# Performance work log

Measured on AMD Instinct MI355X. Metric: run time of the kernel, lower is better.

## Reference

```python
import jax, jax.numpy as jnp
import numpy as np

H = 128; F = 64; G = 50; L = 4; CUT = 10.0
M = 256; K = 8; A = 32
N_TOPO = M * A; N = M * K * A; NCONF = M * K
E_CONF = N * 16; E_GRAPH = N_TOPO * 4
ATOM_TYPES = 100; BOND_TYPES = 10
OFFSETS = jnp.linspace(0.0, CUT, G)
GCOEFF = -0.5 / (CUT / (G - 1)) ** 2  # GaussianSmearing coeff
BN_EPS = 1e-5


def batchnorm(x, g, b):
    # BatchNorm1d in training mode: batch statistics over nodes
    mu = x.mean(0)
    var = ((x - mu) ** 2).mean(0)
    return (x - mu) * jax.lax.rsqrt(var + BN_EPS) * g + b


def setup_inputs():
    key = jax.random.key(0)
    ks = jax.random.split(key, 20)
    s = lambda k, shp: (jax.random.normal(k, shp) * 0.05).astype(jnp.float32)
    inp = {}
    inp["x_topo"] = jax.random.randint(ks[0], (N_TOPO,), 0, ATOM_TYPES)
    inp["pos"] = jax.random.normal(ks[1], (N, 3), dtype=jnp.float32) * 3.0
    inp["edge_index_conf"] = jax.random.randint(ks[2], (2, E_CONF), 0, N)
    inp["edge_index_graph"] = jax.random.randint(ks[3], (2, E_GRAPH), 0, N_TOPO)
    inp["edge_attr_graph"] = jax.random.randint(ks[4], (E_GRAPH,), 0, BOND_TYPES)
    # conf_node_batch: for molecule i, repeat arange(A)+i*A over K conformers
    cnb = (np.arange(M)[:, None, None] * A + np.broadcast_to(np.arange(A), (K, A))).reshape(-1)
    inp["conf_node_batch"] = jnp.asarray(cnb, dtype=jnp.int32)
    inp["pos_batch"] = jnp.repeat(jnp.arange(NCONF), A).astype(jnp.int32)
    inp["conf_batch"] = jnp.repeat(jnp.arange(M), K).astype(jnp.int32)
    # parameters
    inp["atom_emb"] = s(ks[5], (ATOM_TYPES, H))
    inp["cf_lin1_w"] = s(ks[6], (L, H, F))
    inp["cf_mlp_w1"] = s(ks[7], (L, G, F)); inp["cf_mlp_b1"] = jnp.zeros((L, F), jnp.float32)
    inp["cf_mlp_w2"] = s(ks[8], (L, F, F)); inp["cf_mlp_b2"] = jnp.zeros((L, F), jnp.float32)
    inp["cf_lin2_w"] = s(ks[9], (L, F, H)); inp["cf_lin2_b"] = jnp.zeros((L, H), jnp.float32)
    inp["lin_w"] = s(ks[10], (L, H, H)); inp["lin_b"] = jnp.zeros((L, H), jnp.float32)
    inp["bond_emb"] = s(ks[11], (L, BOND_TYPES, H))
    inp["gin_w1"] = s(ks[12], (L, H, H)); inp["gin_b1"] = jnp.zeros((L, H), jnp.float32)
    inp["gin_w2"] = s(ks[13], (L, H, H)); inp["gin_b2"] = jnp.zeros((L, H), jnp.float32)
    inp["gin_bn_g"] = jnp.ones((L, H), jnp.float32); inp["gin_bn_b"] = jnp.zeros((L, H), jnp.float32)
    inp["bn_g"] = jnp.ones((L, H), jnp.float32); inp["bn_b"] = jnp.zeros((L, H), jnp.float32)
    inp["gin_eps"] = jnp.zeros((L,), jnp.float32)
    inp["out_w1"] = s(ks[14], (H, H)); inp["out_b1"] = jnp.zeros((H,), jnp.float32)
    inp["out_w2"] = s(ks[15], (H, 1)); inp["out_b2"] = jnp.zeros((1,), jnp.float32)
    return inp


def _forward(x_topo, edge_index_conf, edge_index_graph, edge_attr_graph,
             conf_node_batch, pos_batch, conf_batch,
             pos, atom_emb, cf_lin1_w, cf_mlp_w1, cf_mlp_b1, cf_mlp_w2, cf_mlp_b2,
             cf_lin2_w, cf_lin2_b, lin_w, lin_b, bond_emb,
             gin_w1, gin_b1, gin_w2, gin_b2, gin_bn_g, gin_bn_b, bn_g, bn_b,
             gin_eps, out_w1, out_b1, out_w2, out_b2):
    # AtomEncoder on topo graph, broadcast to all conformers
    x = atom_emb[x_topo][conf_node_batch]                      # [N, H]
    row, col = edge_index_conf[0], edge_index_conf[1]
    d = pos[row] - pos[col]
    ew = jnp.sqrt(jnp.sum(d * d, axis=-1) + 1e-12)             # edge_weight_conf [E_conf]
    ea = jnp.exp(GCOEFF * (ew[:, None] - OFFSETS) ** 2)        # GaussianSmearing [E_conf, G]
    cwin = 0.5 * (jnp.cos(ew * jnp.pi / CUT) + 1.0)            # SchNet cosine cutoff
    gr, gc = edge_index_graph[0], edge_index_graph[1]
    for l in range(L):
        # CFConv branch (use_conf)
        Wf = (jax.nn.relu(ea @ cf_mlp_w1[l] + cf_mlp_b1[l]) @ cf_mlp_w2[l] + cf_mlp_b2[l]) * cwin[:, None]
        h = x @ cf_lin1_w[l]                                   # lin1, no bias
        agg = jax.ops.segment_sum(h[row] * Wf, col, num_segments=N)
        h = agg @ cf_lin2_w[l] + cf_lin2_b[l]                  # lin2
        h = jax.nn.relu(h)
        h = h @ lin_w[l] + lin_b[l]
        out = x + h                                            # residual
        # GIN branch on topo graph (use_graph)
        x_agg = jax.ops.segment_max(x, conf_node_batch, num_segments=N_TOPO)
        eemb = bond_emb[l][edge_attr_graph]                    # BondEncoder
        magg = jax.ops.segment_sum(jax.nn.relu(x_agg[gr] + eemb), gc, num_segments=N_TOPO)
        hg = (1.0 + gin_eps[l]) * x_agg + magg
        hg = jax.nn.relu(batchnorm(hg @ gin_w1[l] + gin_b1[l], gin_bn_g[l], gin_bn_b[l]))
        hg = hg @ gin_w2[l] + gin_b2[l]
        hg = batchnorm(hg, bn_g[l], bn_b[l])
        out = out + hg[conf_node_batch]
        x = jax.nn.relu(out)
    x = jax.ops.segment_max(x, pos_batch, num_segments=NCONF)  # pool atoms -> conformers
    x = jax.ops.segment_max(x, conf_batch, num_segments=M)     # pool conformers -> molecules
    x = jax.nn.relu(x @ out_w1 + out_b1) @ out_w2 + out_b2     # out_layer
    return x                                                   # training mode: no clamp


def reference(x_topo, pos, edge_index_conf, edge_index_graph, edge_attr_graph,
              conf_node_batch, pos_batch, conf_batch,
              atom_emb, cf_lin1_w, cf_mlp_w1, cf_mlp_b1, cf_mlp_w2, cf_mlp_b2,
              cf_lin2_w, cf_lin2_b, lin_w, lin_b, bond_emb,
              gin_w1, gin_b1, gin_w2, gin_b2, gin_bn_g, gin_bn_b, bn_g, bn_b,
              gin_eps, out_w1, out_b1, out_w2, out_b2):
    return _forward(x_topo, edge_index_conf, edge_index_graph, edge_attr_graph,
                    conf_node_batch, pos_batch, conf_batch,
                    pos, atom_emb, cf_lin1_w, cf_mlp_w1, cf_mlp_b1, cf_mlp_w2, cf_mlp_b2,
                    cf_lin2_w, cf_lin2_b, lin_w, lin_b, bond_emb,
                    gin_w1, gin_b1, gin_w2, gin_b2, gin_bn_g, gin_bn_b, bn_g, bn_b,
                    gin_eps, out_w1, out_b1, out_w2, out_b2)
```

## Files before the change

kernel.cpp:

```cpp
#include <hip/hip_runtime.h>
#include <hip/hip_bf16.h>

#define EC 1048576
#define NN 65536
#define NT 8192
#define MM 256
#define HH 128
#define FF 64
#define GG 50
#define EG 32768

#define TBL 2048
#define TBL_SHIFT 11
#define TRANGE 14.0f

#define CAP 32
#define OVF_CAP 8192
#define NEB (NN * 64 / 256)
#define SEB (8 * (EC / 256))

#define SENT 0xFFE00000

constexpr float STEP = 10.0f / 49.0f;
constexpr float GC = -0.5f / (STEP * STEP);

typedef __attribute__((ext_vector_type(8))) short bf16x8;
typedef __attribute__((ext_vector_type(4))) float f32x4;

__device__ __forceinline__ ushort f2b(float v) {
    __hip_bfloat16 h = __float2bfloat16(v);
    return *(ushort*)&h;
}
__device__ __forceinline__ float b2f(ushort u) {
    return __uint_as_float(((unsigned)u) << 16);
}

#define SETUP_B0 (EC / 256)
#define SETUP_B1 (SETUP_B0 + EG / 256)
#define SETUP_B2 (SETUP_B1 + NN * HH / 8 / 256)
#define SETUP_B3 (SETUP_B2 + NN * CAP / 4 / 256)
__global__ __launch_bounds__(256) void setup_kernel(
    const int* __restrict__ eic, const int* __restrict__ cnb,
    const int* __restrict__ eig, const float* __restrict__ pos,
    const float* __restrict__ emb, const int* __restrict__ xtopo,
    int* __restrict__ degC, ushort* __restrict__ uu16, ushort* __restrict__ xb,
    int4* __restrict__ pay_pad4)
{
    int b = blockIdx.x, tid = threadIdx.x;
    if (b < SETUP_B0) {
        int e = b * 256 + tid;
        int r = eic[e], c = eic[EC + e];
        float dx = pos[r*3+0] - pos[c*3+0];
        float dy = pos[r*3+1] - pos[c*3+1];
        float dz = pos[r*3+2] - pos[c*3+2];
        float w = sqrtf(dx*dx + dy*dy + dz*dz + 1e-12f);
        float u = fminf(w * ((TBL - 1) / TRANGE), 2046.96875f);
        uu16[e] = (ushort)(int)(u * 32.0f);
    } else if (b < SETUP_B1) {
        atomicAdd(&degC[eig[EG + (b - SETUP_B0) * 256 + tid]], 1);
    } else if (b < SETUP_B2) {
        int idx = (b - SETUP_B1) * 256 + tid;
        int n = idx >> 4;
        int f8 = (idx & 15) << 3;
        const float* e = emb + (size_t)xtopo[cnb[n]] * HH + f8;
        float4 v0 = *(const float4*)e;
        float4 v1 = *(const float4*)(e + 4);
        ushort u[8] = {f2b(v0.x), f2b(v0.y), f2b(v0.z), f2b(v0.w),
                       f2b(v1.x), f2b(v1.y), f2b(v1.z), f2b(v1.w)};
        *(bf16x8*)(xb + ((size_t)idx << 3)) = *(const bf16x8*)u;
    } else {
        int idx = (b - SETUP_B2) * 256 + tid;
        pay_pad4[idx] = make_int4(SENT, SENT, SENT, SENT);
    }
}

__global__ __launch_bounds__(256) void scanC_kernel(
    const int* __restrict__ degC, int* __restrict__ offsC, int* __restrict__ curC)
{
    __shared__ int s[256];
    __shared__ int base;
    int tid = threadIdx.x;
    if (tid == 0) base = 0;
    __syncthreads();
    for (int c = 0; c < NT / 256; c++) {
        int v = degC[c * 256 + tid];
        s[tid] = v;
        __syncthreads();
        for (int off = 1; off < 256; off <<= 1) {
            int t = (tid >= off) ? s[tid - off] : 0;
            __syncthreads();
            s[tid] += t;
            __syncthreads();
        }
        int excl = s[tid] - v + base;
        offsC[c * 256 + tid] = excl;
        curC[c * 256 + tid] = excl;
        __syncthreads();
        if (tid == 255) base += s[255];
        __syncthreads();
    }
    if (tid == 0) offsC[NT] = EG;
}

__global__ __launch_bounds__(256) void scatter_all_kernel(
    const int* __restrict__ eic, const ushort* __restrict__ uu16,
    const int* __restrict__ eig, const int* __restrict__ eattr,
    int* __restrict__ cntA, int* __restrict__ curC,
    int* __restrict__ pay_pad, int2* __restrict__ gpay,
    int* __restrict__ ovf_cnt, int2* __restrict__ ovf)
{
    int b = blockIdx.x, tid = threadIdx.x;
    if (b < SEB) {
        int part = b & 7;
        int e = (b >> 3) * 256 + tid;
        int c = eic[EC + e];
        if ((c >> 13) != part) return;
        int pay = ((int)uu16[e] << 16) | (eic[e] & 0xFFFF);
        int slot = atomicAdd(&cntA[c], 1);
        if (slot < CAP) {
            pay_pad[c * CAP + slot] = pay;
        } else {
            int o = atomicAdd(ovf_cnt, 1);
            if (o < OVF_CAP) ovf[o] = make_int2(c, pay);
        }
    } else {
        int e = (b - SEB) * 256 + tid;
        int p = atomicAdd(&curC[eig[EG + e]], 1);
        gpay[p] = make_int2(eig[e], eattr[e]);
    }
}

__global__ __launch_bounds__(64) void build_table_kernel(
    const float* __restrict__ w1a, const float* __restrict__ b1a,
    const float* __restrict__ w2a, const float* __restrict__ b2a,
    float* __restrict__ table_all)
{
    int l = blockIdx.x >> TBL_SHIFT;
    int p = blockIdx.x & (TBL - 1);
    int lane = threadIdx.x;
    const float* w1 = w1a + (size_t)l * GG * FF;
    const float* b1 = b1a + (size_t)l * FF;
    const float* w2 = w2a + (size_t)l * FF * FF;
    const float* b2 = b2a + (size_t)l * FF;
    float w = p * (TRANGE / (TBL - 1));
    float t = b1[lane];
    for (int g = 0; g < GG; g++) {
        float d = w - g * STEP;
        float ea = __expf(GC * d * d);
        t = fmaf(ea, w1[g * 64 + lane], t);
    }
    __shared__ float ts[64];
    ts[lane] = fmaxf(t, 0.f);
    __syncthreads();
    float wf = b2[lane];
    for (int i = 0; i < 64; i++)
        wf = fmaf(ts[i], w2[i * 64 + lane], wf);
    float cw = 0.5f * (__cosf(w * (3.14159265358979323846f / 10.0f)) + 1.0f);
    table_all[((size_t)l * TBL + p) * 64 + lane] = wf * cw;
}

__global__ __launch_bounds__(256) void pack_table_kernel(
    const float* __restrict__ table_all, ushort2* __restrict__ table2_all)
{
    int idx = blockIdx.x * 256 + threadIdx.x;
    int f = idx & 63;
    int rest = idx >> 6;
    int i = rest & (TBL - 1);
    int l = rest >> TBL_SHIFT;
    if (i == TBL - 1) {
        table2_all[idx] = make_ushort2(0, 0);
        return;
    }
    const float* T = table_all + ((size_t)l * TBL) * 64;
    float t0 = T[(size_t)i * 64 + f];
    float t1 = T[(size_t)(i + 1) * 64 + f];
    table2_all[idx] = make_ushort2(f2b(t0), f2b((t1 - t0) * 0.03125f));
}

__device__ __forceinline__ void prep_one(
    const float* __restrict__ W, ushort* __restrict__ Wf, int K, int N, int idx)
{
    int sz = K * N;
    int l = idx / sz;
    int t = idx - l * sz;
    int j = t & 7;
    int lane = (t >> 3) & 63;
    int rest = t >> 9;
    int KTl = K >> 5;
    int kt = rest % KTl;
    int nt = rest / KTl;
    int k = kt * 32 + (lane >> 4) * 8 + j;
    int n = nt * 16 + (lane & 15);
    Wf[idx] = f2b(W[(size_t)l * sz + (size_t)k * N + n]);
}

__global__ __launch_bounds__(256) void prep_all_kernel(
    const float* __restrict__ cf_lin1_w, const float* __restrict__ cf_lin2_w,
    const float* __restrict__ lin_w, const float* __restrict__ gin_w1,
    const float* __restrict__ gin_w2,
    ushort* __restrict__ w1f, ushort* __restrict__ w2f, ushort* __restrict__ wlf,
    ushort* __restrict__ gw1f, ushort* __restrict__ gw2f)
{
    int b = blockIdx.x, tid = threadIdx.x;
    if (b < 128)       prep_one(cf_lin1_w, w1f, HH, FF, b * 256 + tid);
    else if (b < 256)  prep_one(cf_lin2_w, w2f, FF, HH, (b - 128) * 256 + tid);
    else if (b < 512)  prep_one(lin_w, wlf, HH, HH, (b - 256) * 256 + tid);
    else if (b < 768)  prep_one(gin_w1, gw1f, HH, HH, (b - 512) * 256 + tid);
    else               prep_one(gin_w2, gw2f, HH, HH, (b - 768) * 256 + tid);
}

__global__ __launch_bounds__(256) void gemm_bf16_kernel(
    const ushort* __restrict__ A, const ushort* __restrict__ Bf,
    ushort* __restrict__ Cb)
{
    int tid = threadIdx.x;
    int wave = tid >> 6, lane = tid & 63;
    int m0 = (blockIdx.x * 4 + wave) * 16;
    int arow = m0 + (lane & 15);
    int ak = (lane >> 4) * 8;
    bf16x8 a[4];
    const ushort* Ap = A + (size_t)arow * 128 + ak;
    #pragma unroll
    for (int kt = 0; kt < 4; kt++)
        a[kt] = *(const bf16x8*)(Ap + kt * 32);
    f32x4 acc[4];
    #pragma unroll
    for (int i = 0; i < 4; i++) acc[i] = (f32x4){0.f, 0.f, 0.f, 0.f};
    const ushort* Bp = Bf + (size_t)lane * 8;
    #pragma unroll
    for (int nt = 0; nt < 4; nt++)
        #pragma unroll
        for (int kt = 0; kt < 4; kt++) {
            bf16x8 b = *(const bf16x8*)(Bp + ((size_t)(nt * 4 + kt)) * 512);
            acc[nt] = __builtin_amdgcn_mfma_f32_16x16x32_bf16(a[kt], b, acc[nt], 0, 0, 0);
        }
    int col0 = lane & 15;
    int rbase = m0 + (lane >> 4) * 4;
    #pragma unroll
    for (int nt = 0; nt < 4; nt++) {
        int col = nt * 16 + col0;
        #pragma unroll
        for (int r = 0; r < 4; r++)
            Cb[(size_t)(rbase + r) * 64 + col] = f2b(acc[nt][r]);
    }
}

#define EDGE8(BASE) { \
    int pq[8]; \
    { int4 q0 = *(const int4*)(pp + BASE); \
      int4 q1 = *(const int4*)(pp + BASE + 4); \
      pq[0]=__builtin_amdgcn_readfirstlane(q0.x); \
      pq[1]=__builtin_amdgcn_readfirstlane(q0.y); \
      pq[2]=__builtin_amdgcn_readfirstlane(q0.z); \
      pq[3]=__builtin_amdgcn_readfirstlane(q0.w); \
      pq[4]=__builtin_amdgcn_readfirstlane(q1.x); \
      pq[5]=__builtin_amdgcn_readfirstlane(q1.y); \
      pq[6]=__builtin_amdgcn_readfirstlane(q1.z); \
      pq[7]=__builtin_amdgcn_readfirstlane(q1.w); } \
    float h[8]; \
    _Pragma("unroll") \
    for (int q = 0; q < 8; q++) \
        h[q] = b2f(*(const ushort*)(h1c + ((((unsigned)(pq[q] & 0xFFFF)) << 7) + lane2))); \
    unsigned tt[8]; \
    _Pragma("unroll") \
    for (int q = 0; q < 8; q++) \
        tt[q] = *(const unsigned*)(tbc + (((((unsigned)pq[q]) >> 21) << 8) + lane4)); \
    _Pragma("unroll") \
    for (int q = 0; q < 8; q++) { \
        float fr = (float)((unsigned)((pq[q] >> 16) & 31)); \
        float t0 = __uint_as_float(tt[q] << 16); \
        float dts = __uint_as_float(tt[q] & 0xFFFF0000u); \
        float wf = fmaf(dts, fr, t0); \
        if (q & 1) acc1 = fmaf(h[q], wf, acc1); else acc0 = fmaf(h[q], wf, acc0); \
    } }

__global__ __launch_bounds__(256) void edge_xagg_kernel(
    const int* __restrict__ cntA, const int* __restrict__ pay_pad,
    const int* __restrict__ ovf_cnt, const int2* __restrict__ ovf,
    const ushort2* __restrict__ table2, const ushort* __restrict__ h1b,
    ushort* __restrict__ aggb,
    const ushort* __restrict__ xb, ushort* __restrict__ xaggb)
{
    int tid = threadIdx.x;
    if (blockIdx.x < NEB) {
        int lane = tid & 63;
        int node = __builtin_amdgcn_readfirstlane((blockIdx.x * 256 + tid) >> 6);
        unsigned lane2 = (unsigned)lane * 2;
        unsigned lane4 = (unsigned)lane * 4;
        const char* h1c = (const char*)h1b;
        const char* tbc = (const char*)table2;
        int deg = cntA[node];
        int n1 = min(deg, CAP);
        const int* pp = pay_pad + (size_t)node * CAP;
        float acc0 = 0.f, acc1 = 0.f;
        EDGE8(0);
        if (n1 > 8) {
            EDGE8(8);
            if (n1 > 16) {
                EDGE8(16);
                if (n1 > 24) EDGE8(24);
            }
        }
        float acc = acc0 + acc1;
        if (deg > CAP) {
            int no = min(*ovf_cnt, OVF_CAP);
            for (int j = 0; j < no; j++) {
                int2 o = ovf[j];
                if (o.x == node) {
                    unsigned uf = (unsigned)o.y >> 16;
                    int i0 = uf >> 5;
                    float fr = (float)(uf & 31);
                    ushort2 ttv = table2[(size_t)i0 * 64 + lane];
                    acc = fmaf(b2f(h1b[(size_t)(o.y & 0xFFFF) * 64 + lane]),
                               fmaf(b2f(ttv.y), fr, b2f(ttv.x)), acc);
                }
            }
        }
        aggb[(size_t)node * 64 + lane] = f2b(acc);
    } else {
        int idx = (blockIdx.x - NEB) * 256 + tid;
        int tn = idx >> 7, f = idx & 127;
        int m = tn >> 5, a = tn & 31;
        const ushort* base = xb + ((size_t)((m << 8) + a)) * HH + f;
        float mx = -3.4e38f;
        #pragma unroll
        for (int k = 0; k < 8; k++)
            mx = fmaxf(mx, b2f(base[(size_t)(k << 5) * HH]));
        xaggb[idx] = f2b(mx);
    }
}

#define TSTR 136

__global__ __launch_bounds__(256) void gin_gemm1_kernel(
    const int* __restrict__ goffs, const int2* __restrict__ gpay,
    const ushort* __restrict__ xaggb, const float* __restrict__ bemb,
    const float* __restrict__ eps, const ushort* __restrict__ Bf,
    const float* __restrict__ bias, ushort* __restrict__ Cb,
    float* __restrict__ gsum, float* __restrict__ gsq)
{
    __shared__ ushort hg0s[64 * TSTR];
    __shared__ float ssum[128], ssq[128];
    int tid = threadIdx.x;
    if (tid < 128) { ssum[tid] = 0.f; ssq[tid] = 0.f; }
    {
        int row = tid >> 2;
        int fc = (tid & 3) * 32;
        int tn = blockIdx.x * 64 + row;
        float e1 = 1.0f + eps[0];
        float acc[32];
        const ushort* xo = xaggb + (size_t)tn * HH + fc;
        #pragma unroll
        for (int c = 0; c < 4; c++) {
            bf16x8 x = *(const bf16x8*)(xo + c * 8);
            #pragma unroll
            for (int j = 0; j < 8; j++)
                acc[c * 8 + j] = e1 * b2f((ushort)x[j]);
        }
        int beg = goffs[tn], end = goffs[tn + 1];
        for (int p = beg; p < end; p++) {
            int2 g = gpay[p];
            const ushort* xs = xaggb + (size_t)g.x * HH + fc;
            const float* bs = bemb + (size_t)g.y * HH + fc;
            #pragma unroll
            for (int c = 0; c < 4; c++) {
                bf16x8 x = *(const bf16x8*)(xs + c * 8);
                float4 b0 = *(const float4*)(bs + c * 8);
                float4 b1 = *(const float4*)(bs + c * 8 + 4);
                float bb[8] = {b0.x, b0.y, b0.z, b0.w, b1.x, b1.y, b1.z, b1.w};
                #pragma unroll
                for (int j = 0; j < 8; j++)
                    acc[c * 8 + j] += fmaxf(b2f((ushort)x[j]) + bb[j], 0.f);
            }
        }
        ushort* dst = hg0s + row * TSTR + fc;
        #pragma unroll
        for (int j = 0; j < 32; j++) dst[j] = f2b(acc[j]);
    }
    __syncthreads();
    int wave = tid >> 6, lane = tid & 63;
    int lm = lane & 15, lq = lane >> 4;
    int ak = lq * 8;
    bf16x8 a[4];
    #pragma unroll
    for (int kt = 0; kt < 4; kt++)
        a[kt] = *(const bf16x8*)&hg0s[(wave * 16 + lm) * TSTR + ak + kt * 32];
    f32x4 acc[8];
    #pragma unroll
    for (int i = 0; i < 8; i++) acc[i] = (f32x4){0.f, 0.f, 0.f, 0.f};
    const ushort* Bp = Bf + (size_t)lane * 8;
    #pragma unroll
    for (int nt = 0; nt < 8; nt++)
        #pragma unroll
        for (int kt = 0; kt < 4; kt++) {
            bf16x8 b = *(const bf16x8*)(Bp + ((size_t)(nt * 4 + kt)) * 512);
            acc[nt] = __builtin_amdgcn_mfma_f32_16x16x32_bf16(a[kt], b, acc[nt], 0, 0, 0);
        }
    int rbase = blockIdx.x * 64 + wave * 16 + lq * 4;
    #pragma unroll
    for (int nt = 0; nt < 8; nt++) {
        int col = nt * 16 + lm;
        float bs = bias[col];
        float ps = 0.f, pq = 0.f;
        #pragma unroll
        for (int r = 0; r < 4; r++) {
            float v = acc[nt][r] + bs;
            Cb[(size_t)(rbase + r) * 128 + col] = f2b(v);
            ps += v; pq += v * v;
        }
        atomicAdd(&ssum[col], ps);
        atomicAdd(&ssq[col], pq);
    }
    __syncthreads();
    if (tid < 128) {
        atomicAdd(&gsum[tid], ssum[tid]);
        atomicAdd(&gsq[tid], ssq[tid]);
    }
}

__global__ __launch_bounds__(256) void gemm_bn_stats_kernel(
    const ushort* __restrict__ Araw, const float* __restrict__ sum1,
    const float* __restrict__ sq1, const float* __restrict__ g1,
    const float* __restrict__ bb1, const ushort* __restrict__ Bf,
    const float* __restrict__ bias, ushort* __restrict__ Cb,
    float* __restrict__ gsum, float* __restrict__ gsq)
{
    __shared__ float ssum[128], ssq[128];
    int tid = threadIdx.x;
    if (tid < 128) { ssum[tid] = 0.f; ssq[tid] = 0.f; }
    __syncthreads();
    int wave = tid >> 6, lane = tid & 63;
    int m0 = (blockIdx.x * 4 + wave) * 16;
    int arow = m0 + (lane & 15);
    int ak = (lane >> 4) * 8;
    const float INV_NT = 1.0f / NT;
    bf16x8 a[4];
    const ushort* Ap = Araw + (size_t)arow * 128 + ak;
    #pragma unroll
    for (int kt = 0; kt < 4; kt++) {
        bf16x8 raw = *(const bf16x8*)(Ap + kt * 32);
        ushort ub[8];
        #pragma unroll
        for (int j = 0; j < 8; j++) {
            int k = ak + kt * 32 + j;
            float mu = sum1[k] * INV_NT;
            float var = sq1[k] * INV_NT - mu * mu;
            float inv = rsqrtf(var + 1e-5f);
            float w = fmaxf((b2f((ushort)raw[j]) - mu) * inv * g1[k] + bb1[k], 0.f);
            ub[j] = f2b(w);
        }
        a[kt] = *(bf16x8*)ub;
    }
    f32x4 acc[8];
    #pragma unroll
    for (int i = 0; i < 8; i++) acc[i] = (f32x4){0.f, 0.f, 0.f, 0.f};
    const ushort* Bp = Bf + (size_t)lane * 8;
    #pragma unroll
    for (int nt = 0; nt < 8; nt++)
        #pragma unroll
        for (int kt = 0; kt < 4; kt++) {
            bf16x8 b = *(const bf16x8*)(Bp + ((size_t)(nt * 4 + kt)) * 512);
            acc[nt] = __builtin_amdgcn_mfma_f32_16x16x32_bf16(a[kt], b, acc[nt], 0, 0, 0);
        }
    int col0 = lane & 15;
    int rbase = m0 + (lane >> 4) * 4;
    #pragma unroll
    for (int nt = 0; nt < 8; nt++) {
        int col = nt * 16 + col0;
        float bs = bias[col];
        float ps = 0.f, pq = 0.f;
        #pragma unroll
        for (int r = 0; r < 4; r++) {
            float v = acc[nt][r] + bs;
            Cb[(size_t)(rbase + r) * 128 + col] = f2b(v);
            ps += v; pq += v * v;
        }
        atomicAdd(&ssum[col], ps);
        atomicAdd(&ssq[col], pq);
    }
    __syncthreads();
    if (tid < 128) {
        atomicAdd(&gsum[tid], ssum[tid]);
        atomicAdd(&gsq[tid], ssq[tid]);
    }
}

__global__ __launch_bounds__(256) void fused_lin_kernel(
    const ushort* __restrict__ aggb, const ushort* __restrict__ w2,
    const float* __restrict__ b2, const ushort* __restrict__ w3,
    const float* __restrict__ b3, const ushort* __restrict__ hgBb,
    const float* __restrict__ sum2, const float* __restrict__ sq2,
    const float* __restrict__ g2, const float* __restrict__ bb2,
    const int* __restrict__ cnb, const ushort* __restrict__ w1n,
    ushort* __restrict__ xb, ushort* __restrict__ h1b)
{
    __shared__ ushort t1s[4][16 * TSTR];
    __shared__ ushort t2s[4][16 * TSTR];
    int tid = threadIdx.x;
    int wave = tid >> 6, lane = tid & 63;
    int m0 = (blockIdx.x * 4 + wave) * 16;
    int lm = lane & 15;
    int lq = lane >> 4;
    ushort* T1 = t1s[wave];
    ushort* T2 = t2s[wave];
    const float INV_NT = 1.0f / NT;

    const ushort* Ap = aggb + (size_t)(m0 + lm) * 64 + lq * 8;
    bf16x8 a1[2];
    a1[0] = *(const bf16x8*)(Ap);
    a1[1] = *(const bf16x8*)(Ap + 32);
    f32x4 acc[8];
    #pragma unroll
    for (int i = 0; i < 8; i++) acc[i] = (f32x4){0.f, 0.f, 0.f, 0.f};
    {
        const ushort* Bp = w2 + (size_t)lane * 8;
        #pragma unroll
        for (int nt = 0; nt < 8; nt++)
            #pragma unroll
            for (int kt = 0; kt < 2; kt++) {
                bf16x8 b = *(const bf16x8*)(Bp + ((size_t)(nt * 2 + kt)) * 512);
                acc[nt] = __builtin_amdgcn_mfma_f32_16x16x32_bf16(a1[kt], b, acc[nt], 0, 0, 0);
            }
    }
    #pragma unroll
    for (int nt = 0; nt < 8; nt++) {
        int col = nt * 16 + lm;
        float bs = b2[col];
        #pragma unroll
        for (int r = 0; r < 4; r++) {
            float v = fmaxf(acc[nt][r] + bs, 0.f);
            T1[(lq * 4 + r) * TSTR + col] = f2b(v);
        }
    }
    __syncthreads();

    bf16x8 a2[4];
    #pragma unroll
    for (int kt = 0; kt < 4; kt++)
        a2[kt] = *(const bf16x8*)&T1[lm * TSTR + kt * 32 + lq * 8];
    __syncthreads();
    #pragma unroll
    for (int i = 0; i < 4; i++) {
        int idx = i * 64 + lane;
        int row = idx >> 4, ch = idx & 15;
        bf16x8 v = *(const bf16x8*)(xb + (size_t)(m0 + row) * HH + ch * 8);
        *(bf16x8*)&T1[row * TSTR + ch * 8] = v;
    }
    #pragma unroll
    for (int i = 0; i < 8; i++) acc[i] = (f32x4){0.f, 0.f, 0.f, 0.f};
    {
        const ushort* Bp = w3 + (size_t)lane * 8;
        #pragma unroll
        for (int nt = 0; nt < 8; nt++)
            #pragma unroll
            for (int kt = 0; kt < 4; kt++) {
                bf16x8 b = *(const bf16x8*)(Bp + ((size_t)(nt * 4 + kt)) * 512);
                acc[nt] = __builtin_amdgcn_mfma_f32_16x16x32_bf16(a2[kt], b, acc[nt], 0, 0, 0);
            }
    }
    int rbase = m0 + lq * 4;
    int cn[4];
    #pragma unroll
    for (int r = 0; r < 4; r++) cn[r] = cnb[rbase + r];
    #pragma unroll
    for (int nt = 0; nt < 8; nt++) {
        int col = nt * 16 + lm;
        float bs = b3[col];
        float mu2 = sum2[col] * INV_NT;
        float var2 = sq2[col] * INV_NT - mu2 * mu2;
        float sc2 = rsqrtf(var2 + 1e-5f) * g2[col];
        float sh2 = bb2[col] - mu2 * sc2;
        #pragma unroll
        for (int r = 0; r < 4; r++) {
            float v = acc[nt][r] + bs;
            v += b2f(T1[(lq * 4 + r) * TSTR + col]);
            v = fmaf(b2f(hgBb[(size_t)cn[r] * HH + col]), sc2, v + sh2);
            v = fmaxf(v, 0.f);
            T2[(lq * 4 + r) * TSTR + col] = f2b(v);
        }
    }
    __syncthreads();
    #pragma unroll
    for (int i = 0; i < 4; i++) {
        int idx = i * 64 + lane;
        int row = idx >> 4, ch = idx & 15;
        bf16x8 v = *(const bf16x8*)&T2[row * TSTR + ch * 8];
        *(bf16x8*)(xb + (size_t)(m0 + row) * HH + ch * 8) = v;
    }
    if (!w1n) return;
    __syncthreads();

    bf16x8 a3[4];
    #pragma unroll
    for (int kt = 0; kt < 4; kt++)
        a3[kt] = *(const bf16x8*)&T2[lm * TSTR + kt * 32 + lq * 8];
    f32x4 acc3[4];
    #pragma unroll
    for (int i = 0; i < 4; i++) acc3[i] = (f32x4){0.f, 0.f, 0.f, 0.f};
    {
        const ushort* Bp = w1n + (size_t)lane * 8;
        #pragma unroll
        for (int nt = 0; nt < 4; nt++)
            #pragma unroll
            for (int kt = 0; kt < 4; kt++) {
                bf16x8 b = *(const bf16x8*)(Bp + ((size_t)(nt * 4 + kt)) * 512);
                acc3[nt] = __builtin_amdgcn_mfma_f32_16x16x32_bf16(a3[kt], b, acc3[nt], 0, 0, 0);
            }
    }
    #pragma unroll
    for (int nt = 0; nt < 4; nt++) {
        int col = nt * 16 + lm;
        #pragma unroll
        for (int r = 0; r < 4; r++)
            T1[(lq * 4 + r) * TSTR + col] = f2b(acc3[nt][r]);
    }
    __syncthreads();
    #pragma unroll
    for (int i = 0; i < 2; i++) {
        int idx = i * 64 + lane;
        int row = idx >> 3, ch = idx & 7;
        bf16x8 v = *(const bf16x8*)&T1[row * TSTR + ch * 8];
        *(bf16x8*)(h1b + (size_t)(m0 + row) * FF + ch * 8) = v;
    }
}

__global__ __launch_bounds__(128) void out_layer_kernel(
    const ushort* __restrict__ xb, const float* __restrict__ w1,
    const float* __restrict__ b1, const float* __restrict__ w2,
    const float* __restrict__ b2, float* __restrict__ out)
{
    int m = blockIdx.x, f = threadIdx.x;
    const ushort* base = xb + (size_t)m * 256 * HH + f;
    float mx = -3.4e38f;
    for (int r = 0; r < 256; r++)
        mx = fmaxf(mx, b2f(base[(size_t)r * HH]));
    __shared__ float xs[128];
    xs[f] = mx;
    __syncthreads();
    float acc = b1[f];
    for (int k = 0; k < 128; k++) acc = fmaf(xs[k], w1[k * HH + f], acc);
    acc = fmaxf(acc, 0.f) * w2[f];
    __shared__ float red[128];
    red[f] = acc;
    __syncthreads();
    for (int off = 64; off > 0; off >>= 1) {
        if (f < off) red[f] += red[f + off];
        __syncthreads();
    }
    if (f == 0) out[m] = red[0] + b2[0];
}

extern "C" void kernel_launch(void* const* d_in, const int* in_sizes, int n_in,
                              void* d_out, int out_size, void* d_ws, size_t ws_size,
                              hipStream_t stream)
{
    const int*   x_topo    = (const int*)d_in[0];
    const float* pos       = (const float*)d_in[1];
    const int*   eic       = (const int*)d_in[2];
    const int*   eig       = (const int*)d_in[3];
    const int*   eattr     = (const int*)d_in[4];
    const int*   cnb       = (const int*)d_in[5];
    const float* atom_emb  = (const float*)d_in[8];
    const float* cf_lin1_w = (const float*)d_in[9];
    const float* cf_mlp_w1 = (const float*)d_in[10];
    const float* cf_mlp_b1 = (const float*)d_in[11];
    const float* cf_mlp_w2 = (const float*)d_in[12];
    const float* cf_mlp_b2 = (const float*)d_in[13];
    const float* cf_lin2_w = (const float*)d_in[14];
    const float* cf_lin2_b = (const float*)d_in[15];
    const float* lin_w     = (const float*)d_in[16];
    const float* lin_b     = (const float*)d_in[17];
    const float* bond_emb  = (const float*)d_in[18];
    const float* gin_w1    = (const float*)d_in[19];
    const float* gin_b1    = (const float*)d_in[20];
    const float* gin_w2    = (const float*)d_in[21];
    const float* gin_b2    = (const float*)d_in[22];
    const float* gin_bn_g  = (const float*)d_in[23];
    const float* gin_bn_b  = (const float*)d_in[24];
    const float* bn_g      = (const float*)d_in[25];
    const float* bn_b      = (const float*)d_in[26];
    const float* gin_eps   = (const float*)d_in[27];
    const float* out_w1    = (const float*)d_in[28];
    const float* out_b1    = (const float*)d_in[29];
    const float* out_w2    = (const float*)d_in[30];
    const float* out_b2    = (const float*)d_in[31];
    float* out = (float*)d_out;

    char* wsb = (char*)d_ws;
    size_t off = 0;
    auto alloc = [&](size_t nbytes) -> void* {
        void* p = (void*)(wsb + off);
        off += (nbytes + 255) & ~(size_t)255;
        return p;
    };
    ushort* uu16    = (ushort*)alloc(EC * 2);
    ushort* xb      = (ushort*)alloc((size_t)NN * HH * 2);
    ushort* h1b     = (ushort*)alloc((size_t)NN * FF * 2);
    ushort* aggb    = (ushort*)alloc((size_t)NN * FF * 2);
    ushort* xaggb   = (ushort*)alloc((size_t)NT * HH * 2);
    ushort* hgA     = (ushort*)alloc((size_t)NT * HH * 2);
    ushort* hgB     = (ushort*)alloc((size_t)NT * HH * 2);
    float*  table_all  = (float*)alloc((size_t)4 * TBL * 64 * 4);
    ushort2* table2_all = (ushort2*)alloc((size_t)4 * TBL * 64 * 4);
    float*  stats   = (float*)alloc((size_t)4 * 4 * 128 * 4);
    int*    cntA    = (int*)alloc((size_t)NN * 4);
    int*    degC    = (int*)alloc((size_t)NT * 4);
    int*    ovf_cnt = (int*)alloc(256);
    int*    offsC   = (int*)alloc((NT + 1) * 4);
    int*    curC    = (int*)alloc(NT * 4);
    int*    pay_pad = (int*)alloc((size_t)NN * CAP * 4);
    int2*   ovf     = (int2*)alloc((size_t)OVF_CAP * 8);
    int2*   gpay    = (int2*)alloc((size_t)EG * 8);
    ushort* w1f     = (ushort*)alloc((size_t)4 * HH * FF * 2);
    ushort* w2f     = (ushort*)alloc((size_t)4 * FF * HH * 2);
    ushort* wlf     = (ushort*)alloc((size_t)4 * HH * HH * 2);
    ushort* gw1f    = (ushort*)alloc((size_t)4 * HH * HH * 2);
    ushort* gw2f    = (ushort*)alloc((size_t)4 * HH * HH * 2);

    hipMemsetAsync(stats, 0,
        ((size_t)4 * 4 * 128 * 4 + 255 & ~(size_t)255) +
        ((size_t)NN * 4 + 255 & ~(size_t)255) +
        ((size_t)NT * 4 + 255 & ~(size_t)255) + 256, stream);

    setup_kernel<<<SETUP_B3, 256, 0, stream>>>(
        eic, cnb, eig, pos, atom_emb, x_topo, degC, uu16, xb, (int4*)pay_pad);
    scanC_kernel<<<1, 256, 0, stream>>>(degC, offsC, curC);
    scatter_all_kernel<<<SEB + EG / 256, 256, 0, stream>>>(
        eic, uu16, eig, eattr, cntA, curC, pay_pad, gpay, ovf_cnt, ovf);

    build_table_kernel<<<4 * TBL, 64, 0, stream>>>(
        cf_mlp_w1, cf_mlp_b1, cf_mlp_w2, cf_mlp_b2, table_all);
    pack_table_kernel<<<4 * TBL * 64 / 256, 256, 0, stream>>>(table_all, table2_all);
    prep_all_kernel<<<1024, 256, 0, stream>>>(
        cf_lin1_w, cf_lin2_w, lin_w, gin_w1, gin_w2, w1f, w2f, wlf, gw1f, gw2f);

    gemm_bf16_kernel<<<NN / 64, 256, 0, stream>>>(xb, w1f, h1b);

    for (int l = 0; l < 4; l++) {
        const ushort2* table2 = table2_all + (size_t)l * TBL * 64;
        float* sum1 = stats + (size_t)l * 512;
        float* sq1  = sum1 + 128;
        float* sum2 = sum1 + 256;
        float* sq2  = sum1 + 384;
        edge_xagg_kernel<<<NEB + NT * HH / 256, 256, 0, stream>>>(
            cntA, pay_pad, ovf_cnt, ovf, table2, h1b, aggb, xb, xaggb);
        gin_gemm1_kernel<<<NT / 64, 256, 0, stream>>>(
            offsC, gpay, xaggb, bond_emb + (size_t)l * 10 * HH, gin_eps + l,
            gw1f + (size_t)l * HH * HH, gin_b1 + (size_t)l * HH, hgA, sum1, sq1);
        gemm_bn_stats_kernel<<<NT / 64, 256, 0, stream>>>(
            hgA, sum1, sq1, gin_bn_g + (size_t)l * HH, gin_bn_b + (size_t)l * HH,
            gw2f + (size_t)l * HH * HH, gin_b2 + (size_t)l * HH, hgB, sum2, sq2);
        fused_lin_kernel<<<NN / 64, 256, 0, stream>>>(
            aggb, w2f + (size_t)l * FF * HH, cf_lin2_b + (size_t)l * HH,
            wlf + (size_t)l * HH * HH, lin_b + (size_t)l * HH,
            hgB, sum2, sq2, bn_g + (size_t)l * HH, bn_b + (size_t)l * HH,
            cnb, (l < 3) ? (w1f + (size_t)(l + 1) * HH * FF) : nullptr,
            xb, h1b);
    }

    out_layer_kernel<<<MM, 128, 0, stream>>>(xb, out_w1, out_b1, out_w2, out_b2, out);
}
```

Baseline: 632.3 us.

## Fuse conformer edge distance computation with CSR scatter into setup kernel

Computes the packed distance/source payload and scatters it into the padded per-node slots directly inside the setup kernel, so the intermediate uu16 buffer and the partitioned 8x-redundant scatter pass are removed. The sentinel fill of pay_pad moves from setup-kernel blocks to a hipMemsetD32Async issued before setup, which keeps the fill ordered ahead of the scatter. The previous scatter read the edge list eight times and filtered by destination partition, presumably for L2 locality of the atomics. The new path does one unpartitioned pass with scattered atomics across the whole cntA/pay_pad range, and slot order within a node may change.

```diff
diff --git a/kernel.cpp b/kernel.cpp
--- a/kernel.cpp
+++ b/kernel.cpp
@@ -17,7 +17,6 @@
 #define CAP 32
 #define OVF_CAP 8192
 #define NEB (NN * 64 / 256)
-#define SEB (8 * (EC / 256))
 
 #define SENT 0xFFE00000
 
@@ -38,13 +37,13 @@
 #define SETUP_B0 (EC / 256)
 #define SETUP_B1 (SETUP_B0 + EG / 256)
 #define SETUP_B2 (SETUP_B1 + NN * HH / 8 / 256)
-#define SETUP_B3 (SETUP_B2 + NN * CAP / 4 / 256)
 __global__ __launch_bounds__(256) void setup_kernel(
     const int* __restrict__ eic, const int* __restrict__ cnb,
     const int* __restrict__ eig, const float* __restrict__ pos,
     const float* __restrict__ emb, const int* __restrict__ xtopo,
-    int* __restrict__ degC, ushort* __restrict__ uu16, ushort* __restrict__ xb,
-    int4* __restrict__ pay_pad4)
+    int* __restrict__ degC, ushort* __restrict__ xb,
+    int* __restrict__ cntA, int* __restrict__ pay_pad,
+    int* __restrict__ ovf_cnt, int2* __restrict__ ovf)
 {
     int b = blockIdx.x, tid = threadIdx.x;
     if (b < SETUP_B0) {
@@ -55,10 +54,17 @@
         float dz = pos[r*3+2] - pos[c*3+2];
         float w = sqrtf(dx*dx + dy*dy + dz*dz + 1e-12f);
         float u = fminf(w * ((TBL - 1) / TRANGE), 2046.96875f);
-        uu16[e] = (ushort)(int)(u * 32.0f);
+        int pay = (((int)(u * 32.0f)) << 16) | (r & 0xFFFF);
+        int slot = atomicAdd(&cntA[c], 1);
+        if (slot < CAP) {
+            pay_pad[c * CAP + slot] = pay;
+        } else {
+            int o = atomicAdd(ovf_cnt, 1);
+            if (o < OVF_CAP) ovf[o] = make_int2(c, pay);
+        }
     } else if (b < SETUP_B1) {
         atomicAdd(&degC[eig[EG + (b - SETUP_B0) * 256 + tid]], 1);
-    } else if (b < SETUP_B2) {
+    } else {
         int idx = (b - SETUP_B1) * 256 + tid;
         int n = idx >> 4;
         int f8 = (idx & 15) << 3;
@@ -68,9 +74,6 @@
         ushort u[8] = {f2b(v0.x), f2b(v0.y), f2b(v0.z), f2b(v0.w),
                        f2b(v1.x), f2b(v1.y), f2b(v1.z), f2b(v1.w)};
         *(bf16x8*)(xb + ((size_t)idx << 3)) = *(const bf16x8*)u;
-    } else {
-        int idx = (b - SETUP_B2) * 256 + tid;
-        pay_pad4[idx] = make_int4(SENT, SENT, SENT, SENT);
     }
 }
 
@@ -102,32 +105,13 @@
     if (tid == 0) offsC[NT] = EG;
 }
 
-__global__ __launch_bounds__(256) void scatter_all_kernel(
-    const int* __restrict__ eic, const ushort* __restrict__ uu16,
+__global__ __launch_bounds__(256) void scatter_graph_kernel(
     const int* __restrict__ eig, const int* __restrict__ eattr,
-    int* __restrict__ cntA, int* __restrict__ curC,
-    int* __restrict__ pay_pad, int2* __restrict__ gpay,
-    int* __restrict__ ovf_cnt, int2* __restrict__ ovf)
-{
-    int b = blockIdx.x, tid = threadIdx.x;
-    if (b < SEB) {
-        int part = b & 7;
-        int e = (b >> 3) * 256 + tid;
-        int c = eic[EC + e];
-        if ((c >> 13) != part) return;
-        int pay = ((int)uu16[e] << 16) | (eic[e] & 0xFFFF);
-        int slot = atomicAdd(&cntA[c], 1);
-        if (slot < CAP) {
-            pay_pad[c * CAP + slot] = pay;
-        } else {
-            int o = atomicAdd(ovf_cnt, 1);
-            if (o < OVF_CAP) ovf[o] = make_int2(c, pay);
-        }
-    } else {
-        int e = (b - SEB) * 256 + tid;
-        int p = atomicAdd(&curC[eig[EG + e]], 1);
-        gpay[p] = make_int2(eig[e], eattr[e]);
-    }
+    int* __restrict__ curC, int2* __restrict__ gpay)
+{
+    int e = blockIdx.x * 256 + threadIdx.x;
+    int p = atomicAdd(&curC[eig[EG + e]], 1);
+    gpay[p] = make_int2(eig[e], eattr[e]);
 }
 
 __global__ __launch_bounds__(64) void build_table_kernel(
@@ -693,7 +677,6 @@
         off += (nbytes + 255) & ~(size_t)255;
         return p;
     };
-    ushort* uu16    = (ushort*)alloc(EC * 2);
     ushort* xb      = (ushort*)alloc((size_t)NN * HH * 2);
     ushort* h1b     = (ushort*)alloc((size_t)NN * FF * 2);
     ushort* aggb    = (ushort*)alloc((size_t)NN * FF * 2);
@@ -721,12 +704,12 @@
         ((size_t)4 * 4 * 128 * 4 + 255 & ~(size_t)255) +
         ((size_t)NN * 4 + 255 & ~(size_t)255) +
         ((size_t)NT * 4 + 255 & ~(size_t)255) + 256, stream);
-
-    setup_kernel<<<SETUP_B3, 256, 0, stream>>>(
-        eic, cnb, eig, pos, atom_emb, x_topo, degC, uu16, xb, (int4*)pay_pad);
+    hipMemsetD32Async((hipDeviceptr_t)pay_pad, SENT, (size_t)NN * CAP, stream);
+
+    setup_kernel<<<SETUP_B2, 256, 0, stream>>>(
+        eic, cnb, eig, pos, atom_emb, x_topo, degC, xb, cntA, pay_pad, ovf_cnt, ovf);
     scanC_kernel<<<1, 256, 0, stream>>>(degC, offsC, curC);
-    scatter_all_kernel<<<SEB + EG / 256, 256, 0, stream>>>(
-        eic, uu16, eig, eattr, cntA, curC, pay_pad, gpay, ovf_cnt, ovf);
+    scatter_graph_kernel<<<EG / 256, 256, 0, stream>>>(eig, eattr, curC, gpay);
 
     build_table_kernel<<<4 * TBL, 64, 0, stream>>>(
         cf_mlp_w1, cf_mlp_b1, cf_mlp_w2, cf_mlp_b2, table_all);
```

Result: no change. 635.0 us (+0.4%).
